# Performance work log

Measured on AMD Instinct MI355X. Metric: run time of the kernel, lower is better.

Reference implementation:

```python
import jax, jax.numpy as jnp
import numpy as np

N_NODES = 100000
N_EDGES = 3200000
N_GRAPHS = 4096
N_REL = 5
N_BASES = 4
HID = 32


def setup_inputs() -> dict:
    key = jax.random.key(0)
    ks = jax.random.split(key, 32)
    inp = {}
    inp['x'] = jax.random.normal(ks[0], (N_NODES, 4), dtype=jnp.float32)
    inp['edge_index'] = jax.random.randint(ks[1], (2, N_EDGES), 0, N_NODES, dtype=jnp.int64)
    inp['edge_type'] = jax.random.randint(ks[2], (N_EDGES,), 0, N_REL, dtype=jnp.int64)
    inp['user_idx'] = jax.random.randint(ks[3], (N_GRAPHS,), 0, N_NODES, dtype=jnp.int64)
    inp['item_idx'] = jax.random.randint(ks[4], (N_GRAPHS,), 0, N_NODES, dtype=jnp.int64)
    k = 5
    for l in range(4):
        in_c = 4 if l == 0 else HID
        inp[f'basis{l}'] = jax.random.normal(ks[k], (N_BASES, in_c, HID), dtype=jnp.float32) * 0.1; k += 1
        inp[f'comp{l}'] = jax.random.normal(ks[k], (N_REL, N_BASES), dtype=jnp.float32) * 0.5; k += 1
        inp[f'root{l}'] = jax.random.normal(ks[k], (in_c, HID), dtype=jnp.float32) * 0.1; k += 1
        inp[f'bias{l}'] = jax.random.normal(ks[k], (HID,), dtype=jnp.float32) * 0.01; k += 1
    inp['w1'] = jax.random.normal(ks[k], (256, 128), dtype=jnp.float32) * 0.05; k += 1
    inp['b1'] = jnp.zeros((128,), dtype=jnp.float32)
    inp['w2'] = jax.random.normal(ks[k], (128, 1), dtype=jnp.float32) * 0.05; k += 1
    inp['b2'] = jnp.zeros((1,), dtype=jnp.float32)
    return inp


def _rgcn_layer(x, src, key5, inv_cnt, basis, comp, root, bias, n_nodes):
    # mean-aggregate raw source features per (dst, relation): [N, R, in]
    agg = jax.ops.segment_sum(x[src], key5, num_segments=n_nodes * N_REL)
    agg = agg.reshape(n_nodes, N_REL, -1) * inv_cnt
    # basis-decomposed relation weights: W_r = sum_b comp[r,b] * basis[b]
    w = jnp.einsum('rb,bio->rio', comp, basis)  # [R, in, out]
    return jnp.einsum('nri,rio->no', agg, w) + x @ root + bias


def reference(x, edge_index, edge_type, user_idx, item_idx,
              basis0, comp0, root0, bias0,
              basis1, comp1, root1, bias1,
              basis2, comp2, root2, bias2,
              basis3, comp3, root3, bias3,
              w1, b1, w2, b2):
    n_nodes = x.shape[0]
    src, dst = edge_index[0], edge_index[1]
    key5 = dst * N_REL + edge_type  # combined (dst, relation) segment id
    cnt = jax.ops.segment_sum(jnp.ones_like(edge_type, dtype=x.dtype), key5,
                              num_segments=n_nodes * N_REL)
    inv_cnt = (1.0 / jnp.maximum(cnt, 1.0)).reshape(n_nodes, N_REL, 1)
    params = [(basis0, comp0, root0, bias0), (basis1, comp1, root1, bias1),
              (basis2, comp2, root2, bias2), (basis3, comp3, root3, bias3)]
    out = x
    hs = []
    for (basis, comp, root, bias) in params:
        out = jnp.tanh(_rgcn_layer(out, src, key5, inv_cnt, basis, comp, root, bias, n_nodes))
        hs.append(out)
    h = jnp.concatenate(hs, axis=1)            # [N, 128]
    g = jnp.concatenate([h[user_idx], h[item_idx]], axis=1)  # [B, 256]
    z = jax.nn.relu(g @ w1 + b1)
    return (z @ w2 + b2)[:, 0]
```

## Files before the change

### kernel.cpp

```cpp
#include <hip/hip_runtime.h>
#include <hip/hip_bf16.h>
#include <hip/hip_fp16.h>

#define N_NODES 100000
#define N_EDGES 3200000
#define N_GRAPHS 4096
#define N_REL 5
#define N_BASES 4
#define HID 32
#define SEG (N_NODES*N_REL)
#define DUMMY N_NODES

#define NBUCK 196
#define BCAP  20480
#define PBCAP 30720
#define NKEY  2560

typedef _Float16 half8 __attribute__((ext_vector_type(8)));
typedef float floatx4 __attribute__((ext_vector_type(4)));

static __global__ __launch_bounds__(256) void k_part(const int* __restrict__ ei,
                                                     const int* __restrict__ et,
                                                     int* __restrict__ gcur,
                                                     unsigned long long* __restrict__ part) {
    __shared__ int hcnt[NBUCK];
    __shared__ int lbase[NBUCK];
    int t = threadIdx.x;
    if (t < NBUCK) hcnt[t] = 0;
    __syncthreads();
    int e0 = blockIdx.x * 4096;
    int src[16], bkt[16], lkey[16];
#pragma unroll
    for (int j = 0; j < 16; j++) {
        int e = e0 + j * 256 + t;
        if (e < N_EDGES) {
            int s = ei[e];
            int d = ei[N_EDGES + e];
            int r = et[e];
            src[j] = s; bkt[j] = d >> 9; lkey[j] = ((d & 511) * 5) + r;
            atomicAdd(&hcnt[bkt[j]], 1);
        } else bkt[j] = -1;
    }
    __syncthreads();
    if (t < NBUCK) lbase[t] = atomicAdd(&gcur[t], hcnt[t]);
    __syncthreads();
    if (t < NBUCK) hcnt[t] = 0;
    __syncthreads();
#pragma unroll
    for (int j = 0; j < 16; j++) {
        if (bkt[j] >= 0) {
            int rank = atomicAdd(&hcnt[bkt[j]], 1);
            int p = lbase[bkt[j]] + rank;
            if (p < BCAP)
                part[(size_t)bkt[j] * BCAP + p] =
                    ((unsigned long long)(unsigned)lkey[j] << 32) | (unsigned)src[j];
        }
    }
}

static __global__ __launch_bounds__(512) void k_bsort(const unsigned long long* __restrict__ part,
                                                      const int* __restrict__ gcur,
                                                      int* __restrict__ offs,
                                                      int* __restrict__ cnt,
                                                      int* __restrict__ srcs) {
    __shared__ int lhist[NKEY];
    __shared__ int lscan[NKEY];
    __shared__ int sscan[512];
    __shared__ int lsrc[PBCAP];
    int b = blockIdx.x;
    int t = threadIdx.x;
    int n = gcur[b]; if (n > BCAP) n = BCAP;
    const unsigned long long* reg = part + (size_t)b * BCAP;

#pragma unroll
    for (int k = t; k < NKEY; k += 512) lhist[k] = 0;
    __syncthreads();
    for (int i = t; i < n; i += 512)
        atomicAdd(&lhist[(int)(reg[i] >> 32)], 1);
    __syncthreads();

    int loc[5]; int s5 = 0;
#pragma unroll
    for (int j = 0; j < 5; j++) { loc[j] = s5; s5 += (lhist[t * 5 + j] + 7) & ~7; }
    sscan[t] = s5;
    __syncthreads();
    for (int off = 1; off < 512; off <<= 1) {
        int x = (t >= off) ? sscan[t - off] : 0;
        __syncthreads();
        sscan[t] += x;
        __syncthreads();
    }
    int excl = sscan[t] - s5;
#pragma unroll
    for (int j = 0; j < 5; j++) lscan[t * 5 + j] = excl + loc[j];
    __syncthreads();
    int ptot = sscan[511]; if (ptot > PBCAP) ptot = PBCAP;

    int base = b * PBCAP;
#pragma unroll
    for (int j = 0; j < 5; j++) {
        int k = t * 5 + j;
        int segid = b * NKEY + k;
        if (segid < SEG) {
            cnt[segid]  = lhist[k];
            offs[segid] = base + lscan[k];
        }
    }
    __syncthreads();
#pragma unroll
    for (int k = t; k < NKEY; k += 512) lhist[k] = 0;
    for (int i = t; i < ptot; i += 512) lsrc[i] = DUMMY;
    __syncthreads();
    for (int i = t; i < n; i += 512) {
        unsigned long long u = reg[i];
        int k = (int)(u >> 32);
        int pos = lscan[k] + atomicAdd(&lhist[k], 1);
        if (pos < PBCAP) lsrc[pos] = (int)(u & 0xffffffffULL);
    }
    __syncthreads();
    for (int i = t; i < ptot; i += 512) srcs[base + i] = lsrc[i];
}

static __global__ __launch_bounds__(256) void k_pad(const float* __restrict__ x,
                                                    __half* __restrict__ ht0,
                                                    __half* __restrict__ ht1,
                                                    int* __restrict__ srcs) {
    int tid = blockIdx.x * 256 + threadIdx.x;
    if (tid < (N_NODES + 1) * 32) {
        int nd = tid >> 5, ii = tid & 31;
        float v = (nd < N_NODES && ii < 4) ? x[(nd << 2) + ii] : 0.f;
        ht0[tid] = __float2half(v);
    } else {
        int r = tid - (N_NODES + 1) * 32;
        if (r < 32) ht1[N_NODES * 32 + r] = __float2half(0.f);
        else if (r < 48) srcs[NBUCK * PBCAP + (r - 32)] = DUMMY;
    }
}

static __global__ __launch_bounds__(256) void k_wprepB(
    const float* __restrict__ ba0, const float* __restrict__ ro0,
    const float* __restrict__ ba1, const float* __restrict__ ro1,
    const float* __restrict__ ba2, const float* __restrict__ ro2,
    const float* __restrict__ ba3, const float* __restrict__ ro3,
    __half* __restrict__ Wb) {
    int idx = blockIdx.x * 256 + threadIdx.x;
    int j    = idx & 7;
    int lane = (idx >> 3) & 63;
    int tile = (idx >> 9) & 1;
    int ls   = idx >> 10;
    int l    = ls / 5;
    int s    = ls - l * 5;
    const float* basis = (l == 0) ? ba0 : (l == 1) ? ba1 : (l == 2) ? ba2 : ba3;
    const float* root  = (l == 0) ? ro0 : (l == 1) ? ro1 : (l == 2) ? ro2 : ro3;
    int in_c = (l == 0) ? 4 : HID;
    int k = s * 32 + ((lane >> 4) << 3) + j;
    int o = tile * 16 + (lane & 15);
    float v;
    if (k < 128) {
        int b = k >> 5, ii = k & 31;
        v = (ii < in_c) ? basis[(b * in_c + ii) * HID + o] : 0.f;
    } else {
        int ii = k - 128;
        v = (ii < in_c) ? root[ii * HID + o] : 0.f;
    }
    Wb[idx] = __float2half(v);
}

static __global__ __launch_bounds__(256, 6) void k_layer(
    const __half2* __restrict__ tab, const int* __restrict__ offs,
    const int* __restrict__ cnt, const int* __restrict__ srcs,
    const float* __restrict__ comp, const __half* __restrict__ Wbl,
    const float* __restrict__ bias, __half* __restrict__ hout,
    float* __restrict__ hall, int hall_off) {
    __shared__ __align__(16) __half sAgg16[16 * 168];
    int t = threadIdx.x;
    int wave = t >> 6, q = (t >> 4) & 3, p = t & 15;

    float4 cw0 = *(const float4*)(comp + 0);
    float4 cw1 = *(const float4*)(comp + 4);
    float4 cw2 = *(const float4*)(comp + 8);
    float4 cw3 = *(const float4*)(comp + 12);
    float4 cw4 = *(const float4*)(comp + 16);

    int n = blockIdx.x * 16 + wave * 4 + q;
    int s5 = n * N_REL;
    int oo[6], cc[5];
#pragma unroll
    for (int r = 0; r < 5; r++) { oo[r] = offs[s5 + r]; cc[r] = cnt[s5 + r]; }
    oo[5] = oo[4] + ((cc[4] + 7) & ~7);

    __half2 selfh = tab[n * 16 + p];
    float a0x = 0.f, a0y = 0.f, a1x = 0.f, a1y = 0.f;
    float a2x = 0.f, a2y = 0.f, a3x = 0.f, a3y = 0.f;

#pragma unroll
    for (int r = 0; r < 5; r++) {
        int pR = oo[r], pr = oo[r + 1] - pR;
        const int* sp = srcs + pR;
        int4 e0 = *(const int4*)(sp);
        int4 e1 = *(const int4*)(sp + 4);
        __half2 g0 = tab[e0.x * 16 + p], g1 = tab[e0.y * 16 + p];
        __half2 g2 = tab[e0.z * 16 + p], g3 = tab[e0.w * 16 + p];
        __half2 g4 = tab[e1.x * 16 + p], g5 = tab[e1.y * 16 + p];
        __half2 g6 = tab[e1.z * 16 + p], g7 = tab[e1.w * 16 + p];
        __half2 sb = __hadd2(__hadd2(__hadd2(g0, g1), __hadd2(g2, g3)),
                             __hadd2(__hadd2(g4, g5), __hadd2(g6, g7)));
        float2 bf = __half22float2(sb);
        float Sx = bf.x, Sy = bf.y;
        for (int s8 = 8; s8 < pr; s8 += 8) {
            int4 f0 = *(const int4*)(sp + s8);
            int4 f1 = *(const int4*)(sp + s8 + 4);
            __half2 h0 = tab[f0.x * 16 + p], h1 = tab[f0.y * 16 + p];
            __half2 h2 = tab[f0.z * 16 + p], h3 = tab[f0.w * 16 + p];
            __half2 h4 = tab[f1.x * 16 + p], h5 = tab[f1.y * 16 + p];
            __half2 h6 = tab[f1.z * 16 + p], h7 = tab[f1.w * 16 + p];
            __half2 rb = __hadd2(__hadd2(__hadd2(h0, h1), __hadd2(h2, h3)),
                                 __hadd2(__hadd2(h4, h5), __hadd2(h6, h7)));
            float2 rf = __half22float2(rb);
            Sx += rf.x; Sy += rf.y;
        }
        int cr = cc[r];
        float ic = (cr > 0) ? __builtin_amdgcn_rcpf((float)cr) : 0.f;
        float scx = Sx * ic, scy = Sy * ic;
        float4 cw = (r == 0) ? cw0 : (r == 1) ? cw1 : (r == 2) ? cw2
                  : (r == 3) ? cw3 : cw4;
        a0x += cw.x * scx; a0y += cw.x * scy;
        a1x += cw.y * scx; a1y += cw.y * scy;
        a2x += cw.z * scx; a2y += cw.z * scy;
        a3x += cw.w * scx; a3y += cw.w * scy;
    }
    int nl = wave * 4 + q;
    __half2* row = (__half2*)(sAgg16 + nl * 168);
    row[p]      = __float22half2_rn(make_float2(a0x, a0y));
    row[16 + p] = __float22half2_rn(make_float2(a1x, a1y));
    row[32 + p] = __float22half2_rn(make_float2(a2x, a2y));
    row[48 + p] = __float22half2_rn(make_float2(a3x, a3y));
    row[64 + p] = selfh;
    __syncthreads();

    if (wave < 2) {
        int lane = t & 63;
        floatx4 acc = {0.f, 0.f, 0.f, 0.f};
        const __half* aBase = sAgg16 + (lane & 15) * 168 + ((lane >> 4) << 3);
        const __half* bBase = Wbl + wave * 512 + lane * 8;
#pragma unroll
        for (int s = 0; s < 5; s++) {
            half8 a = *(const half8*)(aBase + s * 32);
            half8 b = *(const half8*)(bBase + s * 1024);
            acc = __builtin_amdgcn_mfma_f32_16x16x32_f16(a, b, acc, 0, 0, 0);
        }
        int o = wave * 16 + (lane & 15);
        float bi = bias[o];
#pragma unroll
        for (int r = 0; r < 4; r++) {
            int node = blockIdx.x * 16 + ((lane >> 4) << 2) + r;
            float v = tanhf(acc[r] + bi);
            hall[node * 128 + hall_off + o] = v;
            hout[node * 32 + o] = __float2half(v);
        }
    }
}

static __global__ __launch_bounds__(256) void k_mlp(
    const float* __restrict__ hall, const int* __restrict__ uidx,
    const int* __restrict__ iidx, const float* __restrict__ w1,
    const float* __restrict__ b1, const float* __restrict__ w2,
    const float* __restrict__ b2, float* __restrict__ out) {
    __shared__ float sg[4][4][256];
    int t = threadIdx.x, wave = t >> 6, lane = t & 63;
    int g0 = blockIdx.x * 16 + wave * 4;
#pragma unroll
    for (int gg = 0; gg < 4; gg++) {
        int g = g0 + gg;
        int u = uidx[g], it = iidx[g];
        sg[wave][gg][lane]       = hall[u * 128 + lane];
        sg[wave][gg][64 + lane]  = hall[u * 128 + 64 + lane];
        sg[wave][gg][128 + lane] = hall[it * 128 + lane];
        sg[wave][gg][192 + lane] = hall[it * 128 + 64 + lane];
    }
    __syncthreads();
    float a0[4], a1[4];
#pragma unroll
    for (int gg = 0; gg < 4; gg++) { a0[gg] = b1[lane]; a1[gg] = b1[64 + lane]; }
#pragma unroll 4
    for (int k = 0; k < 256; k++) {
        float wa = w1[k * 128 + lane];
        float wb = w1[k * 128 + 64 + lane];
#pragma unroll
        for (int gg = 0; gg < 4; gg++) {
            float gk = sg[wave][gg][k];
            a0[gg] += gk * wa; a1[gg] += gk * wb;
        }
    }
    float w2a = w2[lane], w2b = w2[64 + lane], bb = b2[0];
#pragma unroll
    for (int gg = 0; gg < 4; gg++) {
        float z0 = fmaxf(a0[gg], 0.f), z1 = fmaxf(a1[gg], 0.f);
        float part = z0 * w2a + z1 * w2b;
#pragma unroll
        for (int off = 32; off > 0; off >>= 1) part += __shfl_xor(part, off);
        if (lane == 0) out[g0 + gg] = part + bb;
    }
}

extern "C" void kernel_launch(void* const* d_in, const int* in_sizes, int n_in,
                              void* d_out, int out_size, void* d_ws, size_t ws_size,
                              hipStream_t stream) {
    const float* x  = (const float*)d_in[0];
    const int*   ei = (const int*)d_in[1];
    const int*   et = (const int*)d_in[2];
    const int*   ui = (const int*)d_in[3];
    const int*   ii = (const int*)d_in[4];
    const float* w1 = (const float*)d_in[21];
    const float* b1 = (const float*)d_in[22];
    const float* w2 = (const float*)d_in[23];
    const float* b2 = (const float*)d_in[24];

    char* ws = (char*)d_ws;
    if (ws_size < 92167680UL) return;
    int*    gcur = (int*)(ws + 0);
    int*    offs = (int*)(ws + 1024);
    int*    cnt  = (int*)(ws + 2001024);
    int*    srcs = (int*)(ws + 4001024);
    __half* ht0  = (__half*)(ws + 28085568);
    __half* ht1  = (__half*)(ws + 34485632);
    __half* Wb   = (__half*)(ws + 40885760);
    float*  hall = (float*)(ws + 40967680);
    unsigned long long* part = (unsigned long long*)hall;

    hipMemsetAsync(gcur, 0, NBUCK * 4, stream);

    k_part<<<782, 256, 0, stream>>>(ei, et, gcur, part);
    k_bsort<<<NBUCK, 512, 0, stream>>>(part, gcur, offs, cnt, srcs);
    k_pad<<<12501, 256, 0, stream>>>(x, ht0, ht1, srcs);
    k_wprepB<<<80, 256, 0, stream>>>(
        (const float*)d_in[5],  (const float*)d_in[7],
        (const float*)d_in[9],  (const float*)d_in[11],
        (const float*)d_in[13], (const float*)d_in[15],
        (const float*)d_in[17], (const float*)d_in[19], Wb);

    __half* tab[2] = {ht0, ht1};
    for (int l = 0; l < 4; l++) {
        const float* comp = (const float*)d_in[6 + 4 * l];
        const float* bias = (const float*)d_in[8 + 4 * l];
        k_layer<<<6250, 256, 0, stream>>>((const __half2*)tab[l & 1], offs, cnt,
                                          srcs, comp, Wb + l * 5120, bias,
                                          tab[(l + 1) & 1], hall, l * 32);
    }
    k_mlp<<<256, 256, 0, stream>>>(hall, ui, ii, w1, b1, w2, b2, (float*)d_out);
}
```

Before: 383.5 us.

## Store layer outputs as fp16 concat table, MFMA MLP, finer partition buckets

```diff
diff --git a/kernel.cpp b/kernel.cpp
--- a/kernel.cpp
+++ b/kernel.cpp
@@ -11,10 +11,10 @@
 #define SEG (N_NODES*N_REL)
 #define DUMMY N_NODES
 
-#define NBUCK 196
-#define BCAP  20480
-#define PBCAP 30720
-#define NKEY  2560
+#define NBUCK 392
+#define BCAP  10240
+#define PBCAP 15360
+#define NKEY  1280
 
 typedef _Float16 half8 __attribute__((ext_vector_type(8)));
 typedef float floatx4 __attribute__((ext_vector_type(4)));
@@ -26,7 +26,7 @@
     __shared__ int hcnt[NBUCK];
     __shared__ int lbase[NBUCK];
     int t = threadIdx.x;
-    if (t < NBUCK) hcnt[t] = 0;
+    for (int k = t; k < NBUCK; k += 256) hcnt[k] = 0;
     __syncthreads();
     int e0 = blockIdx.x * 4096;
     int src[16], bkt[16], lkey[16];
@@ -37,14 +37,14 @@
             int s = ei[e];
             int d = ei[N_EDGES + e];
             int r = et[e];
-            src[j] = s; bkt[j] = d >> 9; lkey[j] = ((d & 511) * 5) + r;
+            src[j] = s; bkt[j] = d >> 8; lkey[j] = ((d & 255) * 5) + r;
             atomicAdd(&hcnt[bkt[j]], 1);
         } else bkt[j] = -1;
     }
     __syncthreads();
-    if (t < NBUCK) lbase[t] = atomicAdd(&gcur[t], hcnt[t]);
-    __syncthreads();
-    if (t < NBUCK) hcnt[t] = 0;
+    for (int k = t; k < NBUCK; k += 256) lbase[k] = atomicAdd(&gcur[k], hcnt[k]);
+    __syncthreads();
+    for (int k = t; k < NBUCK; k += 256) hcnt[k] = 0;
     __syncthreads();
 #pragma unroll
     for (int j = 0; j < 16; j++) {
@@ -65,14 +65,13 @@
                                                       int* __restrict__ srcs) {
     __shared__ int lhist[NKEY];
     __shared__ int lscan[NKEY];
-    __shared__ int sscan[512];
+    __shared__ int sscan[256];
     __shared__ int lsrc[PBCAP];
     int b = blockIdx.x;
     int t = threadIdx.x;
     int n = gcur[b]; if (n > BCAP) n = BCAP;
     const unsigned long long* reg = part + (size_t)b * BCAP;
 
-#pragma unroll
     for (int k = t; k < NKEY; k += 512) lhist[k] = 0;
     __syncthreads();
     for (int i = t; i < n; i += 512)
@@ -80,36 +79,41 @@
     __syncthreads();
 
     int loc[5]; int s5 = 0;
-#pragma unroll
-    for (int j = 0; j < 5; j++) { loc[j] = s5; s5 += (lhist[t * 5 + j] + 7) & ~7; }
-    sscan[t] = s5;
-    __syncthreads();
-    for (int off = 1; off < 512; off <<= 1) {
-        int x = (t >= off) ? sscan[t - off] : 0;
+    if (t < 256) {
+#pragma unroll
+        for (int j = 0; j < 5; j++) { loc[j] = s5; s5 += (lhist[t * 5 + j] + 7) & ~7; }
+        sscan[t] = s5;
+    }
+    __syncthreads();
+    for (int off = 1; off < 256; off <<= 1) {
+        int x = (t >= off && t < 256) ? sscan[t - off] : 0;
         __syncthreads();
-        sscan[t] += x;
+        if (t < 256) sscan[t] += x;
         __syncthreads();
     }
-    int excl = sscan[t] - s5;
-#pragma unroll
-    for (int j = 0; j < 5; j++) lscan[t * 5 + j] = excl + loc[j];
-    __syncthreads();
-    int ptot = sscan[511]; if (ptot > PBCAP) ptot = PBCAP;
+    if (t < 256) {
+        int excl = sscan[t] - s5;
+#pragma unroll
+        for (int j = 0; j < 5; j++) lscan[t * 5 + j] = excl + loc[j];
+    }
+    __syncthreads();
+    int ptot = sscan[255]; if (ptot > PBCAP) ptot = PBCAP;
 
     int base = b * PBCAP;
-#pragma unroll
-    for (int j = 0; j < 5; j++) {
-        int k = t * 5 + j;
-        int segid = b * NKEY + k;
-        if (segid < SEG) {
-            cnt[segid]  = lhist[k];
-            offs[segid] = base + lscan[k];
-        }
-    }
-    __syncthreads();
-#pragma unroll
+    if (t < 256) {
+#pragma unroll
+        for (int j = 0; j < 5; j++) {
+            int k = t * 5 + j;
+            int segid = b * NKEY + k;
+            if (segid < SEG) {
+                cnt[segid]  = lhist[k];
+                offs[segid] = base + lscan[k];
+            }
+        }
+    }
+    __syncthreads();
     for (int k = t; k < NKEY; k += 512) lhist[k] = 0;
-    for (int i = t; i < ptot; i += 512) lsrc[i] = DUMMY;
+    for (int i = t; i < PBCAP; i += 512) lsrc[i] = DUMMY;
     __syncthreads();
     for (int i = t; i < n; i += 512) {
         unsigned long long u = reg[i];
@@ -118,12 +122,12 @@
         if (pos < PBCAP) lsrc[pos] = (int)(u & 0xffffffffULL);
     }
     __syncthreads();
-    for (int i = t; i < ptot; i += 512) srcs[base + i] = lsrc[i];
+    for (int i = t; i < PBCAP; i += 512) srcs[base + i] = lsrc[i];
 }
 
 static __global__ __launch_bounds__(256) void k_pad(const float* __restrict__ x,
                                                     __half* __restrict__ ht0,
-                                                    __half* __restrict__ ht1,
+                                                    __half* __restrict__ hall16,
                                                     int* __restrict__ srcs) {
     int tid = blockIdx.x * 256 + threadIdx.x;
     if (tid < (N_NODES + 1) * 32) {
@@ -132,8 +136,8 @@
         ht0[tid] = __float2half(v);
     } else {
         int r = tid - (N_NODES + 1) * 32;
-        if (r < 32) ht1[N_NODES * 32 + r] = __float2half(0.f);
-        else if (r < 48) srcs[NBUCK * PBCAP + (r - 32)] = DUMMY;
+        if (r < 128) hall16[N_NODES * 128 + r] = __float2half(0.f);
+        else if (r < 144) srcs[NBUCK * PBCAP + (r - 128)] = DUMMY;
     }
 }
 
@@ -166,13 +170,26 @@
     Wb[idx] = __float2half(v);
 }
 
-static __global__ __launch_bounds__(256, 6) void k_layer(
+static __global__ __launch_bounds__(256) void k_wprepM(const float* __restrict__ w1,
+                                                       __half* __restrict__ Wm) {
+    int idx = blockIdx.x * 256 + threadIdx.x;
+    int j    = idx & 7;
+    int lane = (idx >> 3) & 63;
+    int s    = (idx >> 9) & 7;
+    int tile = idx >> 12;
+    int k = s * 32 + ((lane >> 4) << 3) + j;
+    int o = tile * 16 + (lane & 15);
+    Wm[idx] = __float2half(w1[k * 128 + o]);
+}
+
+template <int TSTRIDE>
+static __global__ __launch_bounds__(256, 8) void k_layer(
     const __half2* __restrict__ tab, const int* __restrict__ offs,
     const int* __restrict__ cnt, const int* __restrict__ srcs,
     const float* __restrict__ comp, const __half* __restrict__ Wbl,
-    const float* __restrict__ bias, __half* __restrict__ hout,
-    float* __restrict__ hall, int hall_off) {
-    __shared__ __align__(16) __half sAgg16[16 * 168];
+    const float* __restrict__ bias, __half* __restrict__ hall16, int hall_off) {
+    __shared__ __align__(16) __half sAgg16[16 * 176];
+    constexpr int T2 = TSTRIDE / 2;
     int t = threadIdx.x;
     int wave = t >> 6, q = (t >> 4) & 3, p = t & 15;
 
@@ -189,7 +206,7 @@
     for (int r = 0; r < 5; r++) { oo[r] = offs[s5 + r]; cc[r] = cnt[s5 + r]; }
     oo[5] = oo[4] + ((cc[4] + 7) & ~7);
 
-    __half2 selfh = tab[n * 16 + p];
+    __half2 selfh = tab[n * T2 + p];
     float a0x = 0.f, a0y = 0.f, a1x = 0.f, a1y = 0.f;
     float a2x = 0.f, a2y = 0.f, a3x = 0.f, a3y = 0.f;
 
@@ -199,10 +216,10 @@
         const int* sp = srcs + pR;
         int4 e0 = *(const int4*)(sp);
         int4 e1 = *(const int4*)(sp + 4);
-        __half2 g0 = tab[e0.x * 16 + p], g1 = tab[e0.y * 16 + p];
-        __half2 g2 = tab[e0.z * 16 + p], g3 = tab[e0.w * 16 + p];
-        __half2 g4 = tab[e1.x * 16 + p], g5 = tab[e1.y * 16 + p];
-        __half2 g6 = tab[e1.z * 16 + p], g7 = tab[e1.w * 16 + p];
+        __half2 g0 = tab[e0.x * T2 + p], g1 = tab[e0.y * T2 + p];
+        __half2 g2 = tab[e0.z * T2 + p], g3 = tab[e0.w * T2 + p];
+        __half2 g4 = tab[e1.x * T2 + p], g5 = tab[e1.y * T2 + p];
+        __half2 g6 = tab[e1.z * T2 + p], g7 = tab[e1.w * T2 + p];
         __half2 sb = __hadd2(__hadd2(__hadd2(g0, g1), __hadd2(g2, g3)),
                              __hadd2(__hadd2(g4, g5), __hadd2(g6, g7)));
         float2 bf = __half22float2(sb);
@@ -210,10 +227,10 @@
         for (int s8 = 8; s8 < pr; s8 += 8) {
             int4 f0 = *(const int4*)(sp + s8);
             int4 f1 = *(const int4*)(sp + s8 + 4);
-            __half2 h0 = tab[f0.x * 16 + p], h1 = tab[f0.y * 16 + p];
-            __half2 h2 = tab[f0.z * 16 + p], h3 = tab[f0.w * 16 + p];
-            __half2 h4 = tab[f1.x * 16 + p], h5 = tab[f1.y * 16 + p];
-            __half2 h6 = tab[f1.z * 16 + p], h7 = tab[f1.w * 16 + p];
+            __half2 h0 = tab[f0.x * T2 + p], h1 = tab[f0.y * T2 + p];
+            __half2 h2 = tab[f0.z * T2 + p], h3 = tab[f0.w * T2 + p];
+            __half2 h4 = tab[f1.x * T2 + p], h5 = tab[f1.y * T2 + p];
+            __half2 h6 = tab[f1.z * T2 + p], h7 = tab[f1.w * T2 + p];
             __half2 rb = __hadd2(__hadd2(__hadd2(h0, h1), __hadd2(h2, h3)),
                                  __hadd2(__hadd2(h4, h5), __hadd2(h6, h7)));
             float2 rf = __half22float2(rb);
@@ -230,7 +247,7 @@
         a3x += cw.w * scx; a3y += cw.w * scy;
     }
     int nl = wave * 4 + q;
-    __half2* row = (__half2*)(sAgg16 + nl * 168);
+    __half2* row = (__half2*)(sAgg16 + nl * 176);
     row[p]      = __float22half2_rn(make_float2(a0x, a0y));
     row[16 + p] = __float22half2_rn(make_float2(a1x, a1y));
     row[32 + p] = __float22half2_rn(make_float2(a2x, a2y));
@@ -241,7 +258,7 @@
     if (wave < 2) {
         int lane = t & 63;
         floatx4 acc = {0.f, 0.f, 0.f, 0.f};
-        const __half* aBase = sAgg16 + (lane & 15) * 168 + ((lane >> 4) << 3);
+        const __half* aBase = sAgg16 + (lane & 15) * 176 + ((lane >> 4) << 3);
         const __half* bBase = Wbl + wave * 512 + lane * 8;
 #pragma unroll
         for (int s = 0; s < 5; s++) {
@@ -254,53 +271,59 @@
 #pragma unroll
         for (int r = 0; r < 4; r++) {
             int node = blockIdx.x * 16 + ((lane >> 4) << 2) + r;
-            float v = tanhf(acc[r] + bi);
-            hall[node * 128 + hall_off + o] = v;
-            hout[node * 32 + o] = __float2half(v);
+            hall16[node * 128 + hall_off + o] = __float2half(tanhf(acc[r] + bi));
         }
     }
 }
 
 static __global__ __launch_bounds__(256) void k_mlp(
-    const float* __restrict__ hall, const int* __restrict__ uidx,
-    const int* __restrict__ iidx, const float* __restrict__ w1,
+    const __half* __restrict__ hall16, const int* __restrict__ uidx,
+    const int* __restrict__ iidx, const __half* __restrict__ Wm,
     const float* __restrict__ b1, const float* __restrict__ w2,
     const float* __restrict__ b2, float* __restrict__ out) {
-    __shared__ float sg[4][4][256];
+    __shared__ __align__(16) __half sg[16 * 264];
+    __shared__ float sacc[4][16];
     int t = threadIdx.x, wave = t >> 6, lane = t & 63;
-    int g0 = blockIdx.x * 16 + wave * 4;
-#pragma unroll
-    for (int gg = 0; gg < 4; gg++) {
+    int g0 = blockIdx.x * 16;
+#pragma unroll
+    for (int gg2 = 0; gg2 < 4; gg2++) {
+        int gg = wave * 4 + gg2;
         int g = g0 + gg;
         int u = uidx[g], it = iidx[g];
-        sg[wave][gg][lane]       = hall[u * 128 + lane];
-        sg[wave][gg][64 + lane]  = hall[u * 128 + 64 + lane];
-        sg[wave][gg][128 + lane] = hall[it * 128 + lane];
-        sg[wave][gg][192 + lane] = hall[it * 128 + 64 + lane];
-    }
-    __syncthreads();
-    float a0[4], a1[4];
-#pragma unroll
-    for (int gg = 0; gg < 4; gg++) { a0[gg] = b1[lane]; a1[gg] = b1[64 + lane]; }
-#pragma unroll 4
-    for (int k = 0; k < 256; k++) {
-        float wa = w1[k * 128 + lane];
-        float wb = w1[k * 128 + 64 + lane];
-#pragma unroll
-        for (int gg = 0; gg < 4; gg++) {
-            float gk = sg[wave][gg][k];
-            a0[gg] += gk * wa; a1[gg] += gk * wb;
-        }
-    }
-    float w2a = w2[lane], w2b = w2[64 + lane], bb = b2[0];
-#pragma unroll
-    for (int gg = 0; gg < 4; gg++) {
-        float z0 = fmaxf(a0[gg], 0.f), z1 = fmaxf(a1[gg], 0.f);
-        float part = z0 * w2a + z1 * w2b;
-#pragma unroll
-        for (int off = 32; off > 0; off >>= 1) part += __shfl_xor(part, off);
-        if (lane == 0) out[g0 + gg] = part + bb;
-    }
+        const __half2* hu = (const __half2*)(hall16 + u * 128);
+        const __half2* hi = (const __half2*)(hall16 + it * 128);
+        __half2* dst = (__half2*)(sg + gg * 264);
+        dst[lane]      = hu[lane];
+        dst[64 + lane] = hi[lane];
+    }
+    __syncthreads();
+    floatx4 acc0 = {0.f, 0.f, 0.f, 0.f}, acc1 = {0.f, 0.f, 0.f, 0.f};
+    const __half* aBase = sg + (lane & 15) * 264 + ((lane >> 4) << 3);
+    const __half* bB0 = Wm + (wave * 2 + 0) * 4096 + lane * 8;
+    const __half* bB1 = Wm + (wave * 2 + 1) * 4096 + lane * 8;
+#pragma unroll
+    for (int s = 0; s < 8; s++) {
+        half8 a  = *(const half8*)(aBase + s * 32);
+        half8 f0 = *(const half8*)(bB0 + s * 512);
+        half8 f1 = *(const half8*)(bB1 + s * 512);
+        acc0 = __builtin_amdgcn_mfma_f32_16x16x32_f16(a, f0, acc0, 0, 0, 0);
+        acc1 = __builtin_amdgcn_mfma_f32_16x16x32_f16(a, f1, acc1, 0, 0, 0);
+    }
+    int o0 = wave * 32 + (lane & 15);
+    int o1 = o0 + 16;
+    float b10 = b1[o0], b11 = b1[o1], w20 = w2[o0], w21 = w2[o1];
+#pragma unroll
+    for (int r = 0; r < 4; r++) {
+        float z0 = fmaxf(acc0[r] + b10, 0.f);
+        float z1 = fmaxf(acc1[r] + b11, 0.f);
+        float v = z0 * w20 + z1 * w21;
+#pragma unroll
+        for (int off = 1; off < 16; off <<= 1) v += __shfl_xor(v, off);
+        if ((lane & 15) == 0) sacc[wave][((lane >> 4) << 2) + r] = v;
+    }
+    __syncthreads();
+    if (t < 16)
+        out[g0 + t] = sacc[0][t] + sacc[1][t] + sacc[2][t] + sacc[3][t] + b2[0];
 }
 
 extern "C" void kernel_launch(void* const* d_in, const int* in_sizes, int n_in,
@@ -318,34 +341,38 @@
 
     char* ws = (char*)d_ws;
     if (ws_size < 92167680UL) return;
-    int*    gcur = (int*)(ws + 0);
-    int*    offs = (int*)(ws + 1024);
-    int*    cnt  = (int*)(ws + 2001024);
-    int*    srcs = (int*)(ws + 4001024);
-    __half* ht0  = (__half*)(ws + 28085568);
-    __half* ht1  = (__half*)(ws + 34485632);
-    __half* Wb   = (__half*)(ws + 40885760);
-    float*  hall = (float*)(ws + 40967680);
-    unsigned long long* part = (unsigned long long*)hall;
+    int*    gcur   = (int*)(ws + 0);
+    int*    offs   = (int*)(ws + 2048);
+    int*    cnt    = (int*)(ws + 2002176);
+    int*    srcs   = (int*)(ws + 4002304);
+    __half* ht0    = (__half*)(ws + 28086912);
+    __half* Wb     = (__half*)(ws + 34487040);
+    __half* Wm     = (__half*)(ws + 34528128);
+    __half* hall16 = (__half*)(ws + 34593792);
+    unsigned long long* part = (unsigned long long*)hall16;
 
     hipMemsetAsync(gcur, 0, NBUCK * 4, stream);
 
     k_part<<<782, 256, 0, stream>>>(ei, et, gcur, part);
     k_bsort<<<NBUCK, 512, 0, stream>>>(part, gcur, offs, cnt, srcs);
-    k_pad<<<12501, 256, 0, stream>>>(x, ht0, ht1, srcs);
+    k_pad<<<12501, 256, 0, stream>>>(x, ht0, hall16, srcs);
     k_wprepB<<<80, 256, 0, stream>>>(
         (const float*)d_in[5],  (const float*)d_in[7],
         (const float*)d_in[9],  (const float*)d_in[11],
         (const float*)d_in[13], (const float*)d_in[15],
         (const float*)d_in[17], (const float*)d_in[19], Wb);
-
-    __half* tab[2] = {ht0, ht1};
+    k_wprepM<<<128, 256, 0, stream>>>(w1, Wm);
+
     for (int l = 0; l < 4; l++) {
         const float* comp = (const float*)d_in[6 + 4 * l];
         const float* bias = (const float*)d_in[8 + 4 * l];
-        k_layer<<<6250, 256, 0, stream>>>((const __half2*)tab[l & 1], offs, cnt,
-                                          srcs, comp, Wb + l * 5120, bias,
-                                          tab[(l + 1) & 1], hall, l * 32);
-    }
-    k_mlp<<<256, 256, 0, stream>>>(hall, ui, ii, w1, b1, w2, b2, (float*)d_out);
-}
+        if (l == 0)
+            k_layer<32><<<6250, 256, 0, stream>>>((const __half2*)ht0, offs, cnt,
+                                                  srcs, comp, Wb, bias, hall16, 0);
+        else
+            k_layer<128><<<6250, 256, 0, stream>>>(
+                (const __half2*)(hall16 + (l - 1) * 32), offs, cnt, srcs, comp,
+                Wb + l * 5120, bias, hall16, l * 32);
+    }
+    k_mlp<<<256, 256, 0, stream>>>(hall16, ui, ii, Wm, b1, w2, b2, (float*)d_out);
+}
```

Result: slower. 402.1 us (+4.8%).
